# Performance work log

Measured on AMD Instinct MI355X. Metric: run time of the kernel, lower is better.

The kernel has to match this reference:

```python
import jax, jax.numpy as jnp
import numpy as np

K_NEIGHBORS = 10
SINKHORN_REG = 0.1
SINKHORN_ITERS = 50
EPS = 1e-10


def _pairwise_dist(x):
    # Euclidean cdist; clamp avoids sqrt(0) NaN grads on the diagonal
    sq = jnp.sum(x * x, axis=1)
    d2 = sq[:, None] + sq[None, :] - 2.0 * (x @ x.T)
    return jnp.sqrt(jnp.maximum(d2, 1e-12))


def setup_inputs() -> dict:
    key = jax.random.key(0)
    k1, k2 = jax.random.split(key)
    n, d = 8192, 128
    return {
        "embeddings": jax.random.normal(k1, (n, d), dtype=jnp.float32),
        "reference_embeddings": jax.random.normal(k2, (n, d), dtype=jnp.float32),
    }


def reference(embeddings, reference_embeddings):
    k = min(K_NEIGHBORS, embeddings.shape[0] - 1)

    cur_d = _pairwise_dist(embeddings)              # [n, n]
    ref_d = _pairwise_dist(reference_embeddings)    # [n, n]

    # k+1 smallest (ascending), drop self-distance column
    cur_knn = jnp.sort(cur_d, axis=1)[:, 1:k + 1]   # [n, k]
    ref_knn = jnp.sort(ref_d, axis=1)[:, 1:k + 1]   # [n, k]

    a = cur_knn / (jnp.sum(cur_knn, axis=1, keepdims=True) + EPS)  # [n, k]
    b = ref_knn / (jnp.sum(ref_knn, axis=1, keepdims=True) + EPS)  # [n, k]

    idx = jnp.arange(k, dtype=jnp.float32)
    M = jnp.abs(idx[None, :] - idx[:, None]) / k    # [k, k] shared cost
    Kmat = jnp.exp(-M / SINKHORN_REG)               # [k, k]

    # Batched Sinkhorn across all n samples at once
    def step(u, _):
        v = b / (u @ Kmat + EPS)          # K.T @ u per sample (K symmetric; explicit form u @ K)
        u = a / (v @ Kmat.T + EPS)        # K @ v per sample
        return u, None

    u0 = jnp.ones_like(a)
    u, _ = jax.lax.scan(step, u0, None, length=SINKHORN_ITERS)
    v = b / (u @ Kmat + EPS)

    # sum_ij u_i K_ij M_ij v_j per sample, then mean over n
    per_sample = jnp.einsum('ni,ij,nj->n', u, Kmat * M, v)
    return jnp.mean(per_sample)
```

## Files before the change

### kernel.cpp

```cpp
#include <hip/hip_runtime.h>
#include <hip/hip_bf16.h>
#include <math.h>

#define N 8192
#define D 128
#define NELEM (N * D)
#define KNN 10
#define EPSF 1e-10f
#define RT 32
#define NSLICE 8
#define RH 1024
#define BIGF 3.0e38f

typedef unsigned short ushort_t;
typedef short bf16x8 __attribute__((ext_vector_type(8)));
typedef float f32x4 __attribute__((ext_vector_type(4)));

template <int L>
__device__ __forceinline__ void insM(float (&l)[L], float v) {
  #pragma unroll
  for (int q = L - 1; q >= 1; --q)
    l[q] = __builtin_amdgcn_fmed3f(l[q - 1], l[q], v);
  l[0] = fminf(l[0], v);
}

__global__ void prep_kernel(const float* __restrict__ xc,
                            const float* __restrict__ xr,
                            ushort_t* __restrict__ xb,
                            ushort_t* __restrict__ xa,
                            float* __restrict__ sq) {
  int wid  = (blockIdx.x * blockDim.x + threadIdx.x) >> 6;
  int lane = threadIdx.x & 63;
  if (wid >= 2 * N) return;
  const float* x = (wid < N) ? xc : xr;
  int row = (wid < N) ? wid : wid - N;
  float2 v = *reinterpret_cast<const float2*>(x + (size_t)row * D + lane * 2);
  float s = v.x * v.x + v.y * v.y;
  #pragma unroll
  for (int off = 32; off; off >>= 1) s += __shfl_xor(s, off, 64);
  if (lane == 0) sq[wid] = s;
  auto cvt = [](float f) -> unsigned int {
    unsigned int b = __float_as_uint(f);
    return (b + 0x7FFFu + ((b >> 16) & 1u)) >> 16;
  };
  unsigned int pb = cvt(v.x) | (cvt(v.y) << 16);
  unsigned int pa = cvt(-2.f * v.x) | (cvt(-2.f * v.y) << 16);
  *reinterpret_cast<unsigned int*>(xb + (size_t)wid * D + lane * 2) = pb;
  *reinterpret_cast<unsigned int*>(xa + (size_t)wid * D + lane * 2) = pa;
}

__global__ __launch_bounds__(256, 3) void knn_mfma(
    const ushort_t* __restrict__ xb,
    const ushort_t* __restrict__ xa,
    const float* __restrict__ sq,
    float* __restrict__ partial) {
  __shared__ __align__(16) ushort_t Abuf[2][RT * D];
  __shared__ __align__(16) float SQs[RH];

  const int bid = blockIdx.x;
  const int mat = bid >> 9;
  const int colblk = (bid >> 3) & 63;
  const int slice = bid & 7;
  const ushort_t* __restrict__ XB = xb + (size_t)mat * NELEM;
  const ushort_t* __restrict__ XA = xa + (size_t)mat * NELEM;
  const float* __restrict__ SQ = sq + mat * N;
  const int r0 = slice * RH;
  const int t = threadIdx.x;
  const int w = t >> 6, l = t & 63;
  const int c0w = colblk * 128 + w * 32;

  {
    const float* gs = SQ + r0 + w * 256 + l * 4;
    float* dsts = &SQs[w * 256];
    __builtin_amdgcn_global_load_lds(
        (const __attribute__((address_space(1))) void*)gs,
        (__attribute__((address_space(3))) void*)dsts, 16, 0, 0);
  }

  bf16x8 bfr[2][4];
  #pragma unroll
  for (int j = 0; j < 2; ++j) {
    const ushort_t* p = XB + (size_t)(c0w + j * 16 + (l & 15)) * D + (l >> 4) * 8;
    #pragma unroll
    for (int kk = 0; kk < 4; ++kk)
      bfr[j][kk] = *reinterpret_cast<const bf16x8*>(p + kk * 32);
  }

  float cand[2][KNN];
  #pragma unroll
  for (int j = 0; j < 2; ++j)
    #pragma unroll
    for (int q = 0; q < KNN; ++q) cand[j][q] = BIGF;

  const ushort_t* gbase[2];
  #pragma unroll
  for (int h = 0; h < 2; ++h) {
    const int rg = 2 * w + h;
    const int kk = rg >> 1, ii = rg & 1;
    const int row = ii * 16 + (l & 15);
    const int ch  = kk * 4 + (l >> 4);
    gbase[h] = XA + (size_t)(r0 + row) * D + ch * 8;
  }

  auto stage = [&](int tt, int bb) {
    #pragma unroll
    for (int h = 0; h < 2; ++h) {
      const ushort_t* g = gbase[h] + (size_t)tt * (RT * D);
      ushort_t* dst = &Abuf[bb][(2 * w + h) * 512];
      __builtin_amdgcn_global_load_lds(
          (const __attribute__((address_space(1))) void*)g,
          (__attribute__((address_space(3))) void*)dst, 16, 0, 0);
    }
  };

  stage(0, 0);
  asm volatile("s_waitcnt vmcnt(0)" ::: "memory");
  __syncthreads();

  for (int tt = 0; tt < RH / RT; ++tt) {
    const int cur = tt & 1;
    if (tt < RH / RT - 1) stage(tt + 1, cur ^ 1);

    f32x4 sqi[2];
    #pragma unroll
    for (int i = 0; i < 2; ++i)
      sqi[i] = *reinterpret_cast<const f32x4*>(
          &SQs[tt * RT + i * 16 + ((l >> 4) << 2)]);

    f32x4 acc[2][2];
    #pragma unroll
    for (int i = 0; i < 2; ++i)
      #pragma unroll
      for (int j = 0; j < 2; ++j) acc[i][j] = sqi[i];

    #pragma unroll
    for (int kk = 0; kk < 4; ++kk) {
      bf16x8 af[2];
      #pragma unroll
      for (int i = 0; i < 2; ++i)
        af[i] = *reinterpret_cast<const bf16x8*>(
            &Abuf[cur][(kk * 2 + i) * 512 + l * 8]);
      #pragma unroll
      for (int i = 0; i < 2; ++i)
        #pragma unroll
        for (int j = 0; j < 2; ++j)
          acc[i][j] = __builtin_amdgcn_mfma_f32_16x16x32_bf16(af[i], bfr[j][kk],
                                                              acc[i][j], 0, 0, 0);
    }

    const int rbase = r0 + tt * RT;
    const int idiff = c0w - rbase;
    if ((unsigned)(idiff + 31) < 63u) {
      #pragma unroll
      for (int i = 0; i < 2; ++i)
        #pragma unroll
        for (int j = 0; j < 2; ++j) {
          const int dd = idiff + j * 16 + (l & 15) - i * 16 - ((l >> 4) << 2);
          #pragma unroll
          for (int r = 0; r < 4; ++r)
            if (dd == r) acc[i][j][r] = BIGF;
        }
    }

    #pragma unroll
    for (int r = 0; r < 4; ++r)
      #pragma unroll
      for (int i = 0; i < 2; ++i)
        #pragma unroll
        for (int j = 0; j < 2; ++j)
          insM<KNN>(cand[j], acc[i][j][r]);

    asm volatile("s_waitcnt vmcnt(0)" ::: "memory");
    __syncthreads();
  }

  #pragma unroll
  for (int step = 16; step <= 32; step <<= 1)
    #pragma unroll
    for (int j = 0; j < 2; ++j)
      #pragma unroll
      for (int q = 0; q < KNN; ++q) {
        float o = __shfl_xor(cand[j][q], step, 64);
        insM<KNN>(cand[j], o);
      }

  if (l < 16) {
    #pragma unroll
    for (int j = 0; j < 2; ++j) {
      const int c = c0w + j * 16 + l;
      float* dst = partial + ((size_t)(mat * N + c) * NSLICE + slice) * KNN;
      #pragma unroll
      for (int q = 0; q < KNN; ++q) dst[q] = cand[j][q];
    }
  }
}

__global__ void sink_kernel(const float* __restrict__ partial,
                            const float* __restrict__ sq,
                            float* __restrict__ ps) {
  int s = blockIdx.x * blockDim.x + threadIdx.x;
  if (s >= N) return;
  constexpr float E1 = 0.36787944117144233f;

  float a[KNN], b[KNN];
  #pragma unroll
  for (int m = 0; m < 2; ++m) {
    float best[KNN];
    #pragma unroll
    for (int q = 0; q < KNN; ++q) best[q] = BIGF;
    const float* p = partial + (size_t)(m * N + s) * NSLICE * KNN;
    for (int c = 0; c < NSLICE * KNN; ++c) insM<KNN>(best, p[c]);
    const float sqc = sq[m * N + s];
    float* dst = m ? b : a;
    #pragma unroll
    for (int q = 0; q < KNN; ++q)
      dst[q] = sqrtf(fmaxf(best[q] + sqc, 1e-12f));
  }

  float suma = 0.f, sumb = 0.f;
  #pragma unroll
  for (int q = 0; q < KNN; ++q) { suma += a[q]; sumb += b[q]; }
  float rsa = __builtin_amdgcn_rcpf(suma + EPSF);
  float rsb = __builtin_amdgcn_rcpf(sumb + EPSF);
  #pragma unroll
  for (int q = 0; q < KNN; ++q) { a[q] *= rsa; b[q] *= rsb; }

  float u_[KNN], v_[KNN];
  #pragma unroll
  for (int q = 0; q < KNN; ++q) u_[q] = 1.f;

  #pragma unroll 1
  for (int it = 0; it < 50; ++it) {
    float L[KNN], S[KNN];
    L[0] = u_[0];
    #pragma unroll
    for (int q = 1; q < KNN; ++q) L[q] = fmaf(E1, L[q - 1], u_[q]);
    S[KNN - 1] = u_[KNN - 1];
    #pragma unroll
    for (int q = KNN - 2; q >= 0; --q) S[q] = fmaf(E1, S[q + 1], u_[q]);
    #pragma unroll
    for (int q = 0; q < KNN; ++q) {
      float den = (q < KNN - 1) ? fmaf(E1, S[q + 1], L[q]) : L[KNN - 1];
      v_[q] = b[q] * __builtin_amdgcn_rcpf(den + EPSF);
    }
    L[0] = v_[0];
    #pragma unroll
    for (int q = 1; q < KNN; ++q) L[q] = fmaf(E1, L[q - 1], v_[q]);
    S[KNN - 1] = v_[KNN - 1];
    #pragma unroll
    for (int q = KNN - 2; q >= 0; --q) S[q] = fmaf(E1, S[q + 1], v_[q]);
    #pragma unroll
    for (int q = 0; q < KNN; ++q) {
      float den = (q < KNN - 1) ? fmaf(E1, S[q + 1], L[q]) : L[KNN - 1];
      u_[q] = a[q] * __builtin_amdgcn_rcpf(den + EPSF);
    }
  }
  {
    float L[KNN], S[KNN];
    L[0] = u_[0];
    #pragma unroll
    for (int q = 1; q < KNN; ++q) L[q] = fmaf(E1, L[q - 1], u_[q]);
    S[KNN - 1] = u_[KNN - 1];
    #pragma unroll
    for (int q = KNN - 2; q >= 0; --q) S[q] = fmaf(E1, S[q + 1], u_[q]);
    #pragma unroll
    for (int q = 0; q < KNN; ++q) {
      float den = (q < KNN - 1) ? fmaf(E1, S[q + 1], L[q]) : L[KNN - 1];
      v_[q] = b[q] * __builtin_amdgcn_rcpf(den + EPSF);
    }
  }
  float cost = 0.f;
  #pragma unroll
  for (int i = 0; i < KNN; ++i) {
    float accr = 0.f;
    #pragma unroll
    for (int j = 0; j < KNN; ++j) {
      const int dd = i > j ? i - j : j - i;
      const float wgt = 0.1f * (float)dd * __builtin_expf(-(float)dd);
      accr = fmaf(wgt, v_[j], accr);
    }
    cost = fmaf(u_[i], accr, cost);
  }
  ps[s] = cost;
}

__global__ void reduce_kernel(const float* __restrict__ ps, float* __restrict__ out) {
  __shared__ float red[256];
  int tid = threadIdx.x;
  float s = 0.f;
  for (int i = tid; i < N; i += 256) s += ps[i];
  red[tid] = s;
  __syncthreads();
  #pragma unroll
  for (int off = 128; off > 0; off >>= 1) {
    if (tid < off) red[tid] += red[tid + off];
    __syncthreads();
  }
  if (tid == 0) out[0] = red[0] * (1.0f / N);
}

extern "C" void kernel_launch(void* const* d_in, const int* in_sizes, int n_in,
                              void* d_out, int out_size, void* d_ws, size_t ws_size,
                              hipStream_t stream) {
  const float* xc = (const float*)d_in[0];
  const float* xr = (const float*)d_in[1];
  float* out = (float*)d_out;
  char* wsb = (char*)d_ws;

  float* sq       = (float*)wsb;
  ushort_t* xb    = (ushort_t*)(wsb + (1u << 16));
  ushort_t* xa    = (ushort_t*)(wsb + (1u << 16) + (4u << 20));
  float* partial  = (float*)(wsb + (1u << 16) + (8u << 20));
  float* ps       = partial + (size_t)2 * N * NSLICE * KNN;

  prep_kernel<<<dim3(2 * N / 4), dim3(256), 0, stream>>>(xc, xr, xb, xa, sq);
  knn_mfma<<<dim3(1024), dim3(256), 0, stream>>>(xb, xa, sq, partial);
  sink_kernel<<<dim3(N / 64), dim3(64), 0, stream>>>(partial, sq, ps);
  reduce_kernel<<<dim3(1), dim3(256), 0, stream>>>(ps, out);
}
```

Measured before the change: 115.1 us.

## Stage 64-row tiles per barrier, raise MFMA priority, relax launch bounds

The kNN MFMA kernel now stages 64 rows of A per double-buffer step (two 32-row subtiles), which halves the number of waitcnt and __syncthreads barriers over the row slice. The MFMA section is wrapped in s_setprio raises, and the min-occupancy hint of 3 is dropped from launch bounds so the compiler has more registers to use. The sink kernel launch moves to 256-thread blocks with a quarter as many blocks. Costs: doubled LDS per block and possibly lower occupancy. The sink launch change is safe only if that kernel indexes by global thread id rather than assuming 64-thread blocks.

```diff
diff --git a/kernel.cpp b/kernel.cpp
--- a/kernel.cpp
+++ b/kernel.cpp
@@ -8,6 +8,7 @@
 #define KNN 10
 #define EPSF 1e-10f
 #define RT 32
+#define ST 64
 #define NSLICE 8
 #define RH 1024
 #define BIGF 3.0e38f
@@ -49,12 +50,12 @@
   *reinterpret_cast<unsigned int*>(xa + (size_t)wid * D + lane * 2) = pa;
 }
 
-__global__ __launch_bounds__(256, 3) void knn_mfma(
+__global__ __launch_bounds__(256) void knn_mfma(
     const ushort_t* __restrict__ xb,
     const ushort_t* __restrict__ xa,
     const float* __restrict__ sq,
     float* __restrict__ partial) {
-  __shared__ __align__(16) ushort_t Abuf[2][RT * D];
+  __shared__ __align__(16) ushort_t Abuf[2][ST * D];
   __shared__ __align__(16) float SQs[RH];
 
   const int bid = blockIdx.x;
@@ -102,30 +103,23 @@
     gbase[h] = XA + (size_t)(r0 + row) * D + ch * 8;
   }
 
-  auto stage = [&](int tt, int bb) {
+  auto stage32 = [&](int rowrel, ushort_t* dstbase) {
     #pragma unroll
     for (int h = 0; h < 2; ++h) {
-      const ushort_t* g = gbase[h] + (size_t)tt * (RT * D);
-      ushort_t* dst = &Abuf[bb][(2 * w + h) * 512];
+      const ushort_t* g = gbase[h] + (size_t)rowrel * D;
+      ushort_t* dst = dstbase + (2 * w + h) * 512;
       __builtin_amdgcn_global_load_lds(
           (const __attribute__((address_space(1))) void*)g,
           (__attribute__((address_space(3))) void*)dst, 16, 0, 0);
     }
   };
 
-  stage(0, 0);
-  asm volatile("s_waitcnt vmcnt(0)" ::: "memory");
-  __syncthreads();
-
-  for (int tt = 0; tt < RH / RT; ++tt) {
-    const int cur = tt & 1;
-    if (tt < RH / RT - 1) stage(tt + 1, cur ^ 1);
-
+  auto compute32 = [&](const ushort_t* buf, int rowrel) {
     f32x4 sqi[2];
     #pragma unroll
     for (int i = 0; i < 2; ++i)
       sqi[i] = *reinterpret_cast<const f32x4*>(
-          &SQs[tt * RT + i * 16 + ((l >> 4) << 2)]);
+          &SQs[rowrel + i * 16 + ((l >> 4) << 2)]);
 
     f32x4 acc[2][2];
     #pragma unroll
@@ -133,13 +127,14 @@
       #pragma unroll
       for (int j = 0; j < 2; ++j) acc[i][j] = sqi[i];
 
+    __builtin_amdgcn_s_setprio(1);
     #pragma unroll
     for (int kk = 0; kk < 4; ++kk) {
       bf16x8 af[2];
       #pragma unroll
       for (int i = 0; i < 2; ++i)
         af[i] = *reinterpret_cast<const bf16x8*>(
-            &Abuf[cur][(kk * 2 + i) * 512 + l * 8]);
+            &buf[(kk * 2 + i) * 512 + l * 8]);
       #pragma unroll
       for (int i = 0; i < 2; ++i)
         #pragma unroll
@@ -147,8 +142,9 @@
           acc[i][j] = __builtin_amdgcn_mfma_f32_16x16x32_bf16(af[i], bfr[j][kk],
                                                               acc[i][j], 0, 0, 0);
     }
-
-    const int rbase = r0 + tt * RT;
+    __builtin_amdgcn_s_setprio(0);
+
+    const int rbase = r0 + rowrel;
     const int idiff = c0w - rbase;
     if ((unsigned)(idiff + 31) < 63u) {
       #pragma unroll
@@ -169,7 +165,21 @@
         #pragma unroll
         for (int j = 0; j < 2; ++j)
           insM<KNN>(cand[j], acc[i][j][r]);
-
+  };
+
+  stage32(0, &Abuf[0][0]);
+  stage32(RT, &Abuf[0][RT * D]);
+  asm volatile("s_waitcnt vmcnt(0)" ::: "memory");
+  __syncthreads();
+
+  for (int st = 0; st < RH / ST; ++st) {
+    const int cb = st & 1;
+    if (st < RH / ST - 1) {
+      stage32((st + 1) * ST,      &Abuf[cb ^ 1][0]);
+      stage32((st + 1) * ST + RT, &Abuf[cb ^ 1][RT * D]);
+    }
+    compute32(&Abuf[cb][0],      st * ST);
+    compute32(&Abuf[cb][RT * D], st * ST + RT);
     asm volatile("s_waitcnt vmcnt(0)" ::: "memory");
     __syncthreads();
   }
@@ -315,6 +325,6 @@
 
   prep_kernel<<<dim3(2 * N / 4), dim3(256), 0, stream>>>(xc, xr, xb, xa, sq);
   knn_mfma<<<dim3(1024), dim3(256), 0, stream>>>(xb, xa, sq, partial);
-  sink_kernel<<<dim3(N / 64), dim3(64), 0, stream>>>(partial, sq, ps);
+  sink_kernel<<<dim3(N / 256), dim3(256), 0, stream>>>(partial, sq, ps);
   reduce_kernel<<<dim3(1), dim3(256), 0, stream>>>(ps, out);
 }
```

New measurement: 121.1 us. 5.2% more time.
